# Performance work log

Hardware: AMD Instinct MI355X
Metric: run time of the kernel (lower is better)

Reference implementation:

```python
import jax, jax.numpy as jnp
import numpy as np

N = 50000
E = 1_600_000
IN_C = 128
HID = 64
HEADS = 2
OUT_C = 16
NEG_SLOPE = 0.2
EPS = 1e-16


def setup_inputs() -> dict:
    key = jax.random.key(0)
    ks = jax.random.split(key, 10)
    x = jax.random.normal(ks[0], (N, IN_C), dtype=jnp.float32)
    edge_index = jax.random.randint(ks[1], (2, E), 0, N, dtype=jnp.int64)
    # layer 1: in -> HEADS * HID, concat=True
    s1 = 1.0 / np.sqrt(IN_C)
    W1 = jax.random.normal(ks[2], (IN_C, HEADS * HID), dtype=jnp.float32) * s1
    att_src1 = jax.random.normal(ks[3], (HEADS, HID), dtype=jnp.float32) * (1.0 / np.sqrt(HID))
    att_dst1 = jax.random.normal(ks[4], (HEADS, HID), dtype=jnp.float32) * (1.0 / np.sqrt(HID))
    b1 = jnp.zeros((HEADS * HID,), dtype=jnp.float32)
    # layer 2: HEADS*HID -> OUT_C, heads=1
    s2 = 1.0 / np.sqrt(HEADS * HID)
    W2 = jax.random.normal(ks[5], (HEADS * HID, OUT_C), dtype=jnp.float32) * s2
    att_src2 = jax.random.normal(ks[6], (1, OUT_C), dtype=jnp.float32) * (1.0 / np.sqrt(OUT_C))
    att_dst2 = jax.random.normal(ks[7], (1, OUT_C), dtype=jnp.float32) * (1.0 / np.sqrt(OUT_C))
    b2 = jnp.zeros((OUT_C,), dtype=jnp.float32)
    return {"x": x, "W1": W1, "att_src1": att_src1, "att_dst1": att_dst1, "b1": b1,
            "W2": W2, "att_src2": att_src2, "att_dst2": att_dst2, "b2": b2,
            "edge_index": edge_index}


def gat_conv(x, edge_index, W, att_src, att_dst, bias, heads, out_ch):
    """PyG-style GATConv: per-head linear, additive attention, softmax over
    incoming edges of each destination node, scatter-add aggregation."""
    n = x.shape[0]
    src, dst = edge_index[0], edge_index[1]
    h = (x @ W).reshape(n, heads, out_ch)                # [N,H,C]
    a_src = jnp.einsum('nhc,hc->nh', h, att_src)          # [N,H]
    a_dst = jnp.einsum('nhc,hc->nh', h, att_dst)          # [N,H]
    e = a_src[src] + a_dst[dst]                           # [E,H]
    e = jnp.where(e >= 0, e, NEG_SLOPE * e)               # LeakyReLU(0.2)
    e_max = jax.ops.segment_max(e, dst, num_segments=n)   # [N,H]
    e_max = jax.lax.stop_gradient(jnp.where(jnp.isfinite(e_max), e_max, 0.0))
    e_exp = jnp.exp(e - e_max[dst])                       # [E,H]
    denom = jax.ops.segment_sum(e_exp, dst, num_segments=n)  # [N,H]
    alpha = e_exp / (denom[dst] + EPS)                    # [E,H]
    msg = h[src] * alpha[:, :, None]                      # [E,H,C] (dominant traffic)
    out = jax.ops.segment_sum(msg, dst, num_segments=n)   # [N,H,C]
    return out.reshape(n, heads * out_ch) + bias


def reference(x, W1, att_src1, att_dst1, b1, W2, att_src2, att_dst2, b2, edge_index):
    h = gat_conv(x, edge_index, W1, att_src1, att_dst1, b1, HEADS, HID)
    h = jax.nn.elu(h)
    h = gat_conv(h, edge_index, W2, att_src2, att_dst2, b2, 1, OUT_C)
    return jax.nn.softmax(h, axis=1)
```

## Files before the change

### kernel.cpp

```cpp
#include <hip/hip_runtime.h>
#include <hip/hip_fp16.h>
#include <cstdint>
#include <cstddef>

#define N_NODES 50000
#define N_EDGES 1600000
#define NEG_SLOPE 0.2f
#define GAT_EPS 1e-16f

#define NCHUNK 128
#define CE (N_EDGES / NCHUNK)
#define NBKT 196

typedef _Float16 half8v __attribute__((ext_vector_type(8)));
typedef float f32x4 __attribute__((ext_vector_type(4)));



__global__ __launch_bounds__(256) void k_prep_tiny(
    const float* __restrict__ W1, const float* __restrict__ W2,
    const float* __restrict__ b1,
    _Float16* __restrict__ w1t, float* __restrict__ w2tp, float* __restrict__ b1p) {
    int t = threadIdx.x, b = blockIdx.x;
    if (b < 8) {
        for (int i = t; i < 2048; i += 256) {
            int idx = b * 2048 + i;
            int c = idx >> 7, k = idx & 127;
            w1t[c * 136 + k] = (_Float16)W1[k * 128 + c];
        }
    } else {
        for (int i = t; i < 2176; i += 256) {
            int j = i >> 7, kp = i & 127;
            int real = (kp & 7) * 16 + (kp >> 3);
            w2tp[j * 136 + kp] = W2[real * 16 + j];
        }
        if (t < 128) {
            int real = (t & 7) * 16 + (t >> 3);
            b1p[t] = b1[real];
        }
    }
}


__global__ __launch_bounds__(256) void k_hist(const int* __restrict__ ei,
                                              int* __restrict__ coarse) {
    __shared__ int h[NBKT];
    int t = threadIdx.x, g = blockIdx.x;
    if (t < NBKT) h[t] = 0;
    __syncthreads();
    int e0 = g * CE;
    for (int e = e0 + t; e < e0 + CE; e += 256)
        atomicAdd(&h[ei[N_EDGES + e] >> 8], 1);
    __syncthreads();
    if (t < NBKT) coarse[t * NCHUNK + g] = h[t];
}

__global__ __launch_bounds__(1024) void k_cscan(const int* __restrict__ coarse,
                                                int* __restrict__ cbase,
                                                int* __restrict__ bb,
                                                int* __restrict__ row_start) {
    __shared__ int cl[NBKT * NCHUNK];
    __shared__ int btot[NBKT];
    __shared__ int bbase[NBKT];
    int t = threadIdx.x;
    for (int i = t; i < NBKT * NCHUNK; i += 1024) cl[i] = coarse[i];
    __syncthreads();
    if (t < NBKT) {
        int s = 0;
        for (int g = 0; g < NCHUNK; ++g) s += cl[t * NCHUNK + g];
        btot[t] = s;
    }
    __syncthreads();
    if (t == 0) {
        int base = 0;
        for (int b = 0; b < NBKT; ++b) { bbase[b] = base; base += btot[b]; }
    }
    __syncthreads();
    if (t < NBKT) {
        int run = bbase[t];
        bb[t] = run;
        for (int g = 0; g < NCHUNK; ++g) {
            cbase[t * NCHUNK + g] = run;
            run += cl[t * NCHUNK + g];
        }
    }
    if (t == 0) { bb[NBKT] = N_EDGES; row_start[N_NODES] = N_EDGES; }
}

__global__ __launch_bounds__(256) void k_partition(const int* __restrict__ ei,
                                                   const int* __restrict__ cbase,
                                                   int2* __restrict__ part) {
    __shared__ int loc[NBKT];
    int t = threadIdx.x, g = blockIdx.x;
    if (t < NBKT) loc[t] = cbase[t * NCHUNK + g];
    __syncthreads();
    int e0 = g * CE;
    for (int e = e0 + t; e < e0 + CE; e += 256) {
        int s = ei[e], d = ei[N_EDGES + e];
        int slot = atomicAdd(&loc[d >> 8], 1);
        part[slot] = make_int2(s, d);
    }
}

__global__ __launch_bounds__(256) void k_local(const int2* __restrict__ part,
                                               const int* __restrict__ bb,
                                               const float* __restrict__ a_src1,
                                               const float* __restrict__ a_dst1,
                                               int* __restrict__ row_start,
                                               int4* __restrict__ csr) {
    __shared__ int hist[256];
    __shared__ int fillv[256];
    __shared__ float2 adl[256];
    __shared__ int wtot[4];
    int t = threadIdx.x, b = blockIdx.x;
    int n0 = b << 8;
    int es = bb[b], ee = bb[b + 1];
    hist[t] = 0;
    if (n0 + t < N_NODES) adl[t] = ((const float2*)a_dst1)[n0 + t];
    __syncthreads();
    for (int e = es + t; e < ee; e += 256) atomicAdd(&hist[part[e].y - n0], 1);
    __syncthreads();
    int lane = t & 63, w = t >> 6;
    int v = hist[t], x = v;
#pragma unroll
    for (int off = 1; off < 64; off <<= 1) {
        int y = __shfl_up(x, off, 64);
        if (lane >= off) x += y;
    }
    if (lane == 63) wtot[w] = x;
    __syncthreads();
    int woff = 0;
    for (int i = 0; i < w; ++i) woff += wtot[i];
    int excl = woff + x - v;
    if (n0 + t < N_NODES) row_start[n0 + t] = es + excl;
    fillv[t] = excl;
    __syncthreads();
    for (int e = es + t; e < ee; e += 256) {
        int2 sd = part[e];
        int j = sd.y - n0;
        int slot = es + atomicAdd(&fillv[j], 1);
        float2 as = ((const float2*)a_src1)[sd.x];
        float2 ad = adl[j];
        float e0 = as.x + ad.x; e0 = (e0 >= 0.f) ? e0 : NEG_SLOPE * e0;
        float e1 = as.y + ad.y; e1 = (e1 >= 0.f) ? e1 : NEG_SLOPE * e1;
        csr[slot] = make_int4(sd.x, __float_as_int(expf(e0)), __float_as_int(expf(e1)), 0);
    }
}


__global__ __launch_bounds__(256) void k_gemm1m(
    const float* __restrict__ x, const _Float16* __restrict__ w1t,
    const float* __restrict__ att_src, const float* __restrict__ att_dst,
    _Float16* __restrict__ h1p, float* __restrict__ a_src, float* __restrict__ a_dst) {
    __shared__ _Float16 wl[128 * 136];
    int t = threadIdx.x;
    {
        const uint4* src = (const uint4*)w1t;
        uint4* dst = (uint4*)wl;
        for (int j = t; j < 2176; j += 256) dst[j] = src[j];
    }
    __syncthreads();
    int wv = t >> 6, lane = t & 63;
    int m = lane & 15, q = lane >> 4;
    int nb = blockIdx.x * 64 + wv * 16;
    int grow = nb + m;
    const float* xrow = x + (size_t)((grow < N_NODES) ? grow : (N_NODES - 1)) * 128;
    f32x4 acc[8];
#pragma unroll
    for (int ct = 0; ct < 8; ++ct) acc[ct] = (f32x4){0.f, 0.f, 0.f, 0.f};
#pragma unroll
    for (int kc = 0; kc < 4; ++kc) {
        float4 u0 = *(const float4*)(xrow + kc * 32 + q * 8);
        float4 u1 = *(const float4*)(xrow + kc * 32 + q * 8 + 4);
        half8v a;
        a[0] = (_Float16)u0.x; a[1] = (_Float16)u0.y;
        a[2] = (_Float16)u0.z; a[3] = (_Float16)u0.w;
        a[4] = (_Float16)u1.x; a[5] = (_Float16)u1.y;
        a[6] = (_Float16)u1.z; a[7] = (_Float16)u1.w;
#pragma unroll
        for (int ct = 0; ct < 8; ++ct) {
            half8v bf = *(const half8v*)(wl + (ct * 16 + m) * 136 + kc * 32 + q * 8);
            acc[ct] = __builtin_amdgcn_mfma_f32_16x16x32_f16(a, bf, acc[ct], 0, 0, 0);
        }
    }
    float att_s[8], att_d[8];
#pragma unroll
    for (int ct = 0; ct < 8; ++ct) {
        att_s[ct] = att_src[ct * 16 + m];
        att_d[ct] = att_dst[ct * 16 + m];
    }
#pragma unroll
    for (int r = 0; r < 4; ++r) {
        int gn = nb + q * 4 + r;
        half8v hv;
        float ps0 = 0.f, ps1 = 0.f, pd0 = 0.f, pd1 = 0.f;
#pragma unroll
        for (int ct = 0; ct < 8; ++ct) {
            float v = acc[ct][r];
            hv[ct] = (_Float16)v;
            if (ct < 4) { ps0 += v * att_s[ct]; pd0 += v * att_d[ct]; }
            else        { ps1 += v * att_s[ct]; pd1 += v * att_d[ct]; }
        }
#pragma unroll
        for (int off = 8; off >= 1; off >>= 1) {
            ps0 += __shfl_xor(ps0, off, 64);
            ps1 += __shfl_xor(ps1, off, 64);
            pd0 += __shfl_xor(pd0, off, 64);
            pd1 += __shfl_xor(pd1, off, 64);
        }
        if (gn < N_NODES) {
            *(half8v*)(h1p + (size_t)gn * 128 + m * 8) = hv;
            if (m == 0) {
                a_src[gn * 2 + 0] = ps0;
                a_src[gn * 2 + 1] = ps1;
                a_dst[gn * 2 + 0] = pd0;
                a_dst[gn * 2 + 1] = pd1;
            }
        }
    }
}


__global__ __launch_bounds__(256) void k_agg1f(
    const int* __restrict__ row_start, const int4* __restrict__ csr,
    const _Float16* __restrict__ h1p, const float* __restrict__ b1p,
    const float* __restrict__ w2tp,
    const float* __restrict__ att_src2, const float* __restrict__ att_dst2,
    float* __restrict__ h2, float* __restrict__ as2, float* __restrict__ ad2) {
    __shared__ float w2l[16 * 136];
    __shared__ float rows[4][128];
    int t = threadIdx.x;
    for (int i = t; i < 544; i += 256) ((float4*)w2l)[i] = ((const float4*)w2tp)[i];
    __syncthreads();
    int wv = t >> 6, lane = t & 63;
    int d = blockIdx.x * 4 + wv;
    int row = row_start[d], end = row_start[d + 1];
    int half = lane >> 5;
    int L = lane & 31;
    int c0 = L * 4;
    int head = L & 1;
    float den = 0.f;
    float4 acc = make_float4(0.f, 0.f, 0.f, 0.f);
    int i = row;
    for (; i + 8 <= end; i += 8) {
#pragma unroll
        for (int p = 0; p < 4; ++p) {
            int idx = i + 2 * p + half;
            int4 e4 = csr[idx];
            int s = e4.x;
            float we = head ? __int_as_float(e4.z) : __int_as_float(e4.y);
            uint2 u = *(const uint2*)(h1p + (size_t)s * 128 + c0);
            __half2 p0 = *(__half2*)&u.x;
            __half2 p1 = *(__half2*)&u.y;
            float2 f0 = __half22float2(p0);
            float2 f1 = __half22float2(p1);
            den += we;
            acc.x += we * f0.x; acc.y += we * f0.y;
            acc.z += we * f1.x; acc.w += we * f1.y;
        }
    }
    for (; i < end; i += 2) {
        int idx = i + half;
        bool ok = idx < end;
        int idxc = ok ? idx : i;
        int4 e4 = csr[idxc];
        int s = e4.x;
        float we = head ? __int_as_float(e4.z) : __int_as_float(e4.y);
        if (!ok) we = 0.f;
        uint2 u = *(const uint2*)(h1p + (size_t)s * 128 + c0);
        __half2 p0 = *(__half2*)&u.x;
        __half2 p1 = *(__half2*)&u.y;
        float2 f0 = __half22float2(p0);
        float2 f1 = __half22float2(p1);
        den += we;
        acc.x += we * f0.x; acc.y += we * f0.y;
        acc.z += we * f1.x; acc.w += we * f1.y;
    }
    den += __shfl_xor(den, 32, 64);
    acc.x += __shfl_xor(acc.x, 32, 64);
    acc.y += __shfl_xor(acc.y, 32, 64);
    acc.z += __shfl_xor(acc.z, 32, 64);
    acc.w += __shfl_xor(acc.w, 32, 64);
    float inv = 1.f / (den + GAT_EPS);
    float4 bv = ((const float4*)b1p)[L];
    float o0 = acc.x * inv + bv.x;
    float o1 = acc.y * inv + bv.y;
    float o2 = acc.z * inv + bv.z;
    float o3 = acc.w * inv + bv.w;
    o0 = (o0 > 0.f) ? o0 : expm1f(o0);
    o1 = (o1 > 0.f) ? o1 : expm1f(o1);
    o2 = (o2 > 0.f) ? o2 : expm1f(o2);
    o3 = (o3 > 0.f) ? o3 : expm1f(o3);
    if (half == 0) *(float4*)(&rows[wv][c0]) = make_float4(o0, o1, o2, o3);
    int j = lane & 15, q = lane >> 4;
    const float* r = rows[wv];
    const float* wt = &w2l[j * 136];
    int k0 = q * 32;
    float acc2 = 0.f;
#pragma unroll
    for (int kk = 0; kk < 32; kk += 4) {
        float4 rv = *(const float4*)(r + k0 + kk);
        float4 w4 = *(const float4*)(wt + k0 + kk);
        acc2 += rv.x * w4.x + rv.y * w4.y + rv.z * w4.z + rv.w * w4.w;
    }
    acc2 += __shfl_xor(acc2, 16, 64);
    acc2 += __shfl_xor(acc2, 32, 64);
    if (lane < 16) {
        h2[(size_t)d * 16 + j] = acc2;
        float ps = acc2 * att_src2[j];
        float pd = acc2 * att_dst2[j];
#pragma unroll
        for (int off = 8; off >= 1; off >>= 1) {
            ps += __shfl_xor(ps, off, 64);
            pd += __shfl_xor(pd, off, 64);
        }
        if (lane == 0) { as2[d] = ps; ad2[d] = pd; }
    }
}


__global__ __launch_bounds__(256) void k_agg2(
    const int* __restrict__ row_start, const int4* __restrict__ csr,
    const float* __restrict__ h2, const float* __restrict__ as2,
    const float* __restrict__ ad2, const float* __restrict__ b2,
    float* __restrict__ out) {
    int t = threadIdx.x;
    int wv = t >> 6, lane = t & 63;
    int d = blockIdx.x * 4 + wv;
    int row = row_start[d], end = row_start[d + 1];
    float ad = ad2[d];
    int c = lane & 15, q = lane >> 4;
    float den = 0.f, acc = 0.f;
    for (int base = row; base < end; base += 64) {
        int idx = base + lane;
        float w = 0.f; int s = 0;
        if (idx < end) {
            s = csr[idx].x;
            float e = as2[s] + ad;
            e = (e >= 0.f) ? e : NEG_SLOPE * e;
            w = expf(e);
        }
        den += w;
        int m = end - base; if (m > 64) m = 64;
        for (int jj = 0; jj < m; jj += 4) {
            float wj = __shfl(w, jj + q, 64);
            int sj = __shfl(s, jj + q, 64);
            acc += wj * h2[(size_t)sj * 16 + c];
        }
    }
#pragma unroll
    for (int off = 32; off >= 1; off >>= 1) den += __shfl_xor(den, off, 64);
    acc += __shfl_xor(acc, 16, 64);
    acc += __shfl_xor(acc, 32, 64);
    float v = acc / (den + GAT_EPS) + b2[c];
    float mmax = v;
#pragma unroll
    for (int off = 8; off >= 1; off >>= 1) mmax = fmaxf(mmax, __shfl_xor(mmax, off, 16));
    float ex = expf(v - mmax);
    float sum = ex;
#pragma unroll
    for (int off = 8; off >= 1; off >>= 1) sum += __shfl_xor(sum, off, 16);
    if (lane < 16) out[(size_t)d * 16 + c] = ex / sum;
}


extern "C" void kernel_launch(void* const* d_in, const int* in_sizes, int n_in,
                              void* d_out, int out_size, void* d_ws, size_t ws_size,
                              hipStream_t stream) {
    const float* x        = (const float*)d_in[0];
    const float* W1       = (const float*)d_in[1];
    const float* att_src1 = (const float*)d_in[2];
    const float* att_dst1 = (const float*)d_in[3];
    const float* b1       = (const float*)d_in[4];
    const float* W2       = (const float*)d_in[5];
    const float* att_src2 = (const float*)d_in[6];
    const float* att_dst2 = (const float*)d_in[7];
    const float* b2       = (const float*)d_in[8];
    const int*   ei       = (const int*)d_in[9];

    char* p = (char*)d_ws;
    auto alloc = [&](size_t bytes) {
        char* r = p;
        p += (bytes + 255) & ~(size_t)255;
        return r;
    };
    _Float16* h1p  = (_Float16*)alloc(sizeof(_Float16) * (size_t)N_NODES * 128);
    _Float16* w1t  = (_Float16*)alloc(sizeof(_Float16) * 128 * 136);
    float* w2tp    = (float*)alloc(sizeof(float) * 16 * 136);
    float* b1p     = (float*)alloc(sizeof(float) * 128);
    float* h2      = (float*)alloc(sizeof(float) * (size_t)N_NODES * 16);
    float* a_src   = (float*)alloc(sizeof(float) * N_NODES * 2);
    float* a_dst   = (float*)alloc(sizeof(float) * N_NODES * 2);
    float* as2     = (float*)alloc(sizeof(float) * N_NODES);
    float* ad2     = (float*)alloc(sizeof(float) * N_NODES);
    int* coarse    = (int*)alloc(sizeof(int) * NBKT * NCHUNK);
    int* cbase     = (int*)alloc(sizeof(int) * NBKT * NCHUNK);
    int* bb        = (int*)alloc(sizeof(int) * (NBKT + 1));
    int* row_start = (int*)alloc(sizeof(int) * (N_NODES + 1));
    int2* part     = (int2*)alloc(sizeof(int2) * (size_t)N_EDGES);
    int4* csr      = (int4*)alloc(sizeof(int4) * (size_t)N_EDGES);

    k_prep_tiny<<<9, 256, 0, stream>>>(W1, W2, b1, w1t, w2tp, b1p);
    k_gemm1m<<<782, 256, 0, stream>>>(x, w1t, att_src1, att_dst1, h1p, a_src, a_dst);
    k_hist<<<NCHUNK, 256, 0, stream>>>(ei, coarse);
    k_cscan<<<1, 1024, 0, stream>>>(coarse, cbase, bb, row_start);
    k_partition<<<NCHUNK, 256, 0, stream>>>(ei, cbase, part);
    k_local<<<NBKT, 256, 0, stream>>>(part, bb, a_src, a_dst, row_start, csr);
    k_agg1f<<<N_NODES / 4, 256, 0, stream>>>(row_start, csr, h1p, b1p, w2tp, att_src2, att_dst2, h2, as2, ad2);
    k_agg2<<<N_NODES / 4, 256, 0, stream>>>(row_start, csr, h2, as2, ad2, b2, (float*)d_out);
}
```

Baseline: 278.7 us.

## Merge GEMM and histogram kernels, pad W2 stride, unroll layer-2 gather

The layer-1 GEMM and the edge-destination histogram now run in one launch, with extra blocks branching into the histogram path. This removes a kernel launch and lets the two independent stages overlap. The W2 shared-memory stride changes from 136 to 132, and the dot-product start offset is rotated per quarter-wave to cut LDS bank conflicts. The layer-2 aggregation loop is unrolled to issue two gathers per iteration, at the cost of a few more registers.

```diff
diff --git a/kernel.cpp b/kernel.cpp
--- a/kernel.cpp
+++ b/kernel.cpp
@@ -11,6 +11,7 @@
 #define NCHUNK 128
 #define CE (N_EDGES / NCHUNK)
 #define NBKT 196
+#define GEMM_BLOCKS 782
 
 typedef _Float16 half8v __attribute__((ext_vector_type(8)));
 typedef float f32x4 __attribute__((ext_vector_type(4)));
@@ -29,10 +30,14 @@
             w1t[c * 136 + k] = (_Float16)W1[k * 128 + c];
         }
     } else {
-        for (int i = t; i < 2176; i += 256) {
-            int j = i >> 7, kp = i & 127;
-            int real = (kp & 7) * 16 + (kp >> 3);
-            w2tp[j * 136 + kp] = W2[real * 16 + j];
+        for (int i = t; i < 2112; i += 256) {
+            int j = i / 132, kp = i % 132;
+            if (kp < 128) {
+                int real = (kp & 7) * 16 + (kp >> 3);
+                w2tp[j * 132 + kp] = W2[real * 16 + j];
+            } else {
+                w2tp[j * 132 + kp] = 0.f;
+            }
         }
         if (t < 128) {
             int real = (t & 7) * 16 + (t >> 3);
@@ -42,18 +47,93 @@
 }
 
 
-__global__ __launch_bounds__(256) void k_hist(const int* __restrict__ ei,
-                                              int* __restrict__ coarse) {
-    __shared__ int h[NBKT];
-    int t = threadIdx.x, g = blockIdx.x;
-    if (t < NBKT) h[t] = 0;
-    __syncthreads();
-    int e0 = g * CE;
-    for (int e = e0 + t; e < e0 + CE; e += 256)
-        atomicAdd(&h[ei[N_EDGES + e] >> 8], 1);
-    __syncthreads();
-    if (t < NBKT) coarse[t * NCHUNK + g] = h[t];
-}
+__global__ __launch_bounds__(256) void k_gh(
+    const float* __restrict__ x, const _Float16* __restrict__ w1t,
+    const float* __restrict__ att_src, const float* __restrict__ att_dst,
+    _Float16* __restrict__ h1p, float* __restrict__ a_src, float* __restrict__ a_dst,
+    const int* __restrict__ ei, int* __restrict__ coarse) {
+    __shared__ __align__(16) char smem[34816];
+    int t = threadIdx.x;
+    int b = blockIdx.x;
+    if (b >= GEMM_BLOCKS) {
+        int* h = (int*)smem;
+        int g = b - GEMM_BLOCKS;
+        if (t < NBKT) h[t] = 0;
+        __syncthreads();
+        int e0 = g * CE;
+        for (int e = e0 + t; e < e0 + CE; e += 256)
+            atomicAdd(&h[ei[N_EDGES + e] >> 8], 1);
+        __syncthreads();
+        if (t < NBKT) coarse[t * NCHUNK + g] = h[t];
+        return;
+    }
+    _Float16* wl = (_Float16*)smem;
+    {
+        const uint4* src = (const uint4*)w1t;
+        uint4* dst = (uint4*)wl;
+        for (int j = t; j < 2176; j += 256) dst[j] = src[j];
+    }
+    __syncthreads();
+    int wv = t >> 6, lane = t & 63;
+    int m = lane & 15, q = lane >> 4;
+    int nb = b * 64 + wv * 16;
+    int grow = nb + m;
+    const float* xrow = x + (size_t)((grow < N_NODES) ? grow : (N_NODES - 1)) * 128;
+    f32x4 acc[8];
+#pragma unroll
+    for (int ct = 0; ct < 8; ++ct) acc[ct] = (f32x4){0.f, 0.f, 0.f, 0.f};
+#pragma unroll
+    for (int kc = 0; kc < 4; ++kc) {
+        float4 u0 = *(const float4*)(xrow + kc * 32 + q * 8);
+        float4 u1 = *(const float4*)(xrow + kc * 32 + q * 8 + 4);
+        half8v a;
+        a[0] = (_Float16)u0.x; a[1] = (_Float16)u0.y;
+        a[2] = (_Float16)u0.z; a[3] = (_Float16)u0.w;
+        a[4] = (_Float16)u1.x; a[5] = (_Float16)u1.y;
+        a[6] = (_Float16)u1.z; a[7] = (_Float16)u1.w;
+#pragma unroll
+        for (int ct = 0; ct < 8; ++ct) {
+            half8v bf = *(const half8v*)(wl + (ct * 16 + m) * 136 + kc * 32 + q * 8);
+            acc[ct] = __builtin_amdgcn_mfma_f32_16x16x32_f16(a, bf, acc[ct], 0, 0, 0);
+        }
+    }
+    float att_s[8], att_d[8];
+#pragma unroll
+    for (int ct = 0; ct < 8; ++ct) {
+        att_s[ct] = att_src[ct * 16 + m];
+        att_d[ct] = att_dst[ct * 16 + m];
+    }
+#pragma unroll
+    for (int r = 0; r < 4; ++r) {
+        int gn = nb + q * 4 + r;
+        half8v hv;
+        float ps0 = 0.f, ps1 = 0.f, pd0 = 0.f, pd1 = 0.f;
+#pragma unroll
+        for (int ct = 0; ct < 8; ++ct) {
+            float v = acc[ct][r];
+            hv[ct] = (_Float16)v;
+            if (ct < 4) { ps0 += v * att_s[ct]; pd0 += v * att_d[ct]; }
+            else        { ps1 += v * att_s[ct]; pd1 += v * att_d[ct]; }
+        }
+#pragma unroll
+        for (int off = 8; off >= 1; off >>= 1) {
+            ps0 += __shfl_xor(ps0, off, 64);
+            ps1 += __shfl_xor(ps1, off, 64);
+            pd0 += __shfl_xor(pd0, off, 64);
+            pd1 += __shfl_xor(pd1, off, 64);
+        }
+        if (gn < N_NODES) {
+            *(half8v*)(h1p + (size_t)gn * 128 + m * 8) = hv;
+            if (m == 0) {
+                a_src[gn * 2 + 0] = ps0;
+                a_src[gn * 2 + 1] = ps1;
+                a_dst[gn * 2 + 0] = pd0;
+                a_dst[gn * 2 + 1] = pd1;
+            }
+        }
+    }
+}
+
 
 __global__ __launch_bounds__(1024) void k_cscan(const int* __restrict__ coarse,
                                                 int* __restrict__ cbase,
@@ -148,89 +228,16 @@
 }
 
 
-__global__ __launch_bounds__(256) void k_gemm1m(
-    const float* __restrict__ x, const _Float16* __restrict__ w1t,
-    const float* __restrict__ att_src, const float* __restrict__ att_dst,
-    _Float16* __restrict__ h1p, float* __restrict__ a_src, float* __restrict__ a_dst) {
-    __shared__ _Float16 wl[128 * 136];
-    int t = threadIdx.x;
-    {
-        const uint4* src = (const uint4*)w1t;
-        uint4* dst = (uint4*)wl;
-        for (int j = t; j < 2176; j += 256) dst[j] = src[j];
-    }
-    __syncthreads();
-    int wv = t >> 6, lane = t & 63;
-    int m = lane & 15, q = lane >> 4;
-    int nb = blockIdx.x * 64 + wv * 16;
-    int grow = nb + m;
-    const float* xrow = x + (size_t)((grow < N_NODES) ? grow : (N_NODES - 1)) * 128;
-    f32x4 acc[8];
-#pragma unroll
-    for (int ct = 0; ct < 8; ++ct) acc[ct] = (f32x4){0.f, 0.f, 0.f, 0.f};
-#pragma unroll
-    for (int kc = 0; kc < 4; ++kc) {
-        float4 u0 = *(const float4*)(xrow + kc * 32 + q * 8);
-        float4 u1 = *(const float4*)(xrow + kc * 32 + q * 8 + 4);
-        half8v a;
-        a[0] = (_Float16)u0.x; a[1] = (_Float16)u0.y;
-        a[2] = (_Float16)u0.z; a[3] = (_Float16)u0.w;
-        a[4] = (_Float16)u1.x; a[5] = (_Float16)u1.y;
-        a[6] = (_Float16)u1.z; a[7] = (_Float16)u1.w;
-#pragma unroll
-        for (int ct = 0; ct < 8; ++ct) {
-            half8v bf = *(const half8v*)(wl + (ct * 16 + m) * 136 + kc * 32 + q * 8);
-            acc[ct] = __builtin_amdgcn_mfma_f32_16x16x32_f16(a, bf, acc[ct], 0, 0, 0);
-        }
-    }
-    float att_s[8], att_d[8];
-#pragma unroll
-    for (int ct = 0; ct < 8; ++ct) {
-        att_s[ct] = att_src[ct * 16 + m];
-        att_d[ct] = att_dst[ct * 16 + m];
-    }
-#pragma unroll
-    for (int r = 0; r < 4; ++r) {
-        int gn = nb + q * 4 + r;
-        half8v hv;
-        float ps0 = 0.f, ps1 = 0.f, pd0 = 0.f, pd1 = 0.f;
-#pragma unroll
-        for (int ct = 0; ct < 8; ++ct) {
-            float v = acc[ct][r];
-            hv[ct] = (_Float16)v;
-            if (ct < 4) { ps0 += v * att_s[ct]; pd0 += v * att_d[ct]; }
-            else        { ps1 += v * att_s[ct]; pd1 += v * att_d[ct]; }
-        }
-#pragma unroll
-        for (int off = 8; off >= 1; off >>= 1) {
-            ps0 += __shfl_xor(ps0, off, 64);
-            ps1 += __shfl_xor(ps1, off, 64);
-            pd0 += __shfl_xor(pd0, off, 64);
-            pd1 += __shfl_xor(pd1, off, 64);
-        }
-        if (gn < N_NODES) {
-            *(half8v*)(h1p + (size_t)gn * 128 + m * 8) = hv;
-            if (m == 0) {
-                a_src[gn * 2 + 0] = ps0;
-                a_src[gn * 2 + 1] = ps1;
-                a_dst[gn * 2 + 0] = pd0;
-                a_dst[gn * 2 + 1] = pd1;
-            }
-        }
-    }
-}
-
-
 __global__ __launch_bounds__(256) void k_agg1f(
     const int* __restrict__ row_start, const int4* __restrict__ csr,
     const _Float16* __restrict__ h1p, const float* __restrict__ b1p,
     const float* __restrict__ w2tp,
     const float* __restrict__ att_src2, const float* __restrict__ att_dst2,
     float* __restrict__ h2, float* __restrict__ as2, float* __restrict__ ad2) {
-    __shared__ float w2l[16 * 136];
+    __shared__ float w2l[16 * 132];
     __shared__ float rows[4][128];
     int t = threadIdx.x;
-    for (int i = t; i < 544; i += 256) ((float4*)w2l)[i] = ((const float4*)w2tp)[i];
+    for (int i = t; i < 528; i += 256) ((float4*)w2l)[i] = ((const float4*)w2tp)[i];
     __syncthreads();
     int wv = t >> 6, lane = t & 63;
     int d = blockIdx.x * 4 + wv;
@@ -294,13 +301,14 @@
     if (half == 0) *(float4*)(&rows[wv][c0]) = make_float4(o0, o1, o2, o3);
     int j = lane & 15, q = lane >> 4;
     const float* r = rows[wv];
-    const float* wt = &w2l[j * 136];
+    const float* wt = &w2l[j * 132];
     int k0 = q * 32;
     float acc2 = 0.f;
 #pragma unroll
-    for (int kk = 0; kk < 32; kk += 4) {
-        float4 rv = *(const float4*)(r + k0 + kk);
-        float4 w4 = *(const float4*)(wt + k0 + kk);
+    for (int sI = 0; sI < 8; ++sI) {
+        int sp = ((sI + q) & 7) * 4;
+        float4 rv = *(const float4*)(r + k0 + sp);
+        float4 w4 = *(const float4*)(wt + k0 + sp);
         acc2 += rv.x * w4.x + rv.y * w4.y + rv.z * w4.z + rv.w * w4.w;
     }
     acc2 += __shfl_xor(acc2, 16, 64);
@@ -342,7 +350,17 @@
         }
         den += w;
         int m = end - base; if (m > 64) m = 64;
-        for (int jj = 0; jj < m; jj += 4) {
+        int jj = 0;
+        for (; jj + 8 <= m; jj += 8) {
+            float w0 = __shfl(w, jj + q, 64);
+            int   s0 = __shfl(s, jj + q, 64);
+            float w1_ = __shfl(w, jj + 4 + q, 64);
+            int   s1 = __shfl(s, jj + 4 + q, 64);
+            float h0 = h2[(size_t)s0 * 16 + c];
+            float h1_ = h2[(size_t)s1 * 16 + c];
+            acc += w0 * h0 + w1_ * h1_;
+        }
+        for (; jj < m; jj += 4) {
             float wj = __shfl(w, jj + q, 64);
             int sj = __shfl(s, jj + q, 64);
             acc += wj * h2[(size_t)sj * 16 + c];
@@ -386,7 +404,7 @@
     };
     _Float16* h1p  = (_Float16*)alloc(sizeof(_Float16) * (size_t)N_NODES * 128);
     _Float16* w1t  = (_Float16*)alloc(sizeof(_Float16) * 128 * 136);
-    float* w2tp    = (float*)alloc(sizeof(float) * 16 * 136);
+    float* w2tp    = (float*)alloc(sizeof(float) * 16 * 132);
     float* b1p     = (float*)alloc(sizeof(float) * 128);
     float* h2      = (float*)alloc(sizeof(float) * (size_t)N_NODES * 16);
     float* a_src   = (float*)alloc(sizeof(float) * N_NODES * 2);
@@ -401,8 +419,7 @@
     int4* csr      = (int4*)alloc(sizeof(int4) * (size_t)N_EDGES);
 
     k_prep_tiny<<<9, 256, 0, stream>>>(W1, W2, b1, w1t, w2tp, b1p);
-    k_gemm1m<<<782, 256, 0, stream>>>(x, w1t, att_src1, att_dst1, h1p, a_src, a_dst);
-    k_hist<<<NCHUNK, 256, 0, stream>>>(ei, coarse);
+    k_gh<<<GEMM_BLOCKS + NCHUNK, 256, 0, stream>>>(x, w1t, att_src1, att_dst1, h1p, a_src, a_dst, ei, coarse);
     k_cscan<<<1, 1024, 0, stream>>>(coarse, cbase, bb, row_start);
     k_partition<<<NCHUNK, 256, 0, stream>>>(ei, cbase, part);
     k_local<<<NBKT, 256, 0, stream>>>(part, bb, a_src, a_dst, row_start, csr);
```

Result: faster. 267.2 us (-4.1%).
